# Kernel tuning notes

Hardware: AMD Instinct MI355X
Metric: run time of the kernel (lower is better)

## Reference

```python
import jax, jax.numpy as jnp
import numpy as np

B, T, I = 2048, 256, 64   # batch, seq_len, n_input
H = 128                   # n_lstm_hidden
K = 128                   # n_KDN_hidden
O = 64                    # n_output


def setup_inputs() -> dict:
    key = jax.random.key(0)
    ks = jax.random.split(key, 16)
    def xavier(k, shape):
        fan_in, fan_out = shape[1], shape[0]
        std = np.sqrt(2.0 / (fan_in + fan_out))
        return jax.random.normal(k, shape, dtype=jnp.float32) * std
    inp = {
        'x': jax.random.normal(ks[0], (B, T, I), dtype=jnp.float32),
        # LSTMCell 1 (input I -> hidden H); PyTorch gate order i,f,g,o
        'W_ih1': xavier(ks[1], (4 * H, I)),
        'W_hh1': xavier(ks[2], (4 * H, H)),
        'b_ih1': jnp.zeros((4 * H,), jnp.float32),
        'b_hh1': jnp.zeros((4 * H,), jnp.float32),
        # LSTMCell 2 (H -> H)
        'W_ih2': xavier(ks[3], (4 * H, H)),
        'W_hh2': xavier(ks[4], (4 * H, H)),
        'b_ih2': jnp.zeros((4 * H,), jnp.float32),
        'b_hh2': jnp.zeros((4 * H,), jnp.float32),
        # KDN: 6 Linear layers (H+I)->K, K->K x4, K->O
        'Wk0': xavier(ks[5], (K, H + I)), 'bk0': jnp.zeros((K,), jnp.float32),
        'Wk1': xavier(ks[6], (K, K)),     'bk1': jnp.zeros((K,), jnp.float32),
        'Wk2': xavier(ks[7], (K, K)),     'bk2': jnp.zeros((K,), jnp.float32),
        'Wk3': xavier(ks[8], (K, K)),     'bk3': jnp.zeros((K,), jnp.float32),
        'Wk4': xavier(ks[9], (K, K)),     'bk4': jnp.zeros((K,), jnp.float32),
        'Wk5': xavier(ks[10], (O, K)),    'bk5': jnp.zeros((O,), jnp.float32),
    }
    return inp


def _lstm_cell(x_t, h, c, W_ih, W_hh, b_ih, b_hh):
    # PyTorch LSTMCell math; gates ordered i, f, g, o
    gates = x_t @ W_ih.T + h @ W_hh.T + (b_ih + b_hh)
    i, f, g, o = jnp.split(gates, 4, axis=-1)
    i = jax.nn.sigmoid(i)
    f = jax.nn.sigmoid(f)
    g = jnp.tanh(g)
    o = jax.nn.sigmoid(o)
    c_new = f * c + i * g
    h_new = o * jnp.tanh(c_new)
    return h_new, c_new


def reference(x, W_ih1, W_hh1, b_ih1, b_hh1, W_ih2, W_hh2, b_ih2, b_hh2,
              Wk0, bk0, Wk1, bk1, Wk2, bk2, Wk3, bk3, Wk4, bk4, Wk5, bk5):
    Bx = x.shape[0]
    h1 = jnp.zeros((Bx, H), x.dtype)
    c1 = jnp.zeros((Bx, H), x.dtype)
    h2 = jnp.zeros((Bx, H), x.dtype)
    c2 = jnp.zeros((Bx, H), x.dtype)

    xs = jnp.swapaxes(x, 0, 1)  # [T, B, I] for scan over time

    def step(carry, x_t):
        h1, c1, h2, c2 = carry
        h1, c1 = _lstm_cell(x_t, h1, c1, W_ih1, W_hh1, b_ih1, b_hh1)
        # Dropout is identity in eval mode
        h2, c2 = _lstm_cell(h1, h2, c2, W_ih2, W_hh2, b_ih2, b_hh2)
        return (h1, c1, h2, c2), None

    (h1, c1, h2, c2), _ = jax.lax.scan(step, (h1, c1, h2, c2), xs)

    r = jnp.concatenate([h2, x[:, -1, :]], axis=1)  # [B, H+I]
    y = r
    for W, b in ((Wk0, bk0), (Wk1, bk1), (Wk2, bk2), (Wk3, bk3), (Wk4, bk4)):
        y = jax.nn.relu(y @ W.T + b)
    y = y @ Wk5.T + bk5  # final Linear, no activation
    return (y, h2, r)
```

## Files before the change

kernel.cpp:

```cpp
#include <hip/hip_runtime.h>
#include <cstddef>


typedef __attribute__((ext_vector_type(8))) short short8;
typedef __attribute__((ext_vector_type(4))) float float4v;

#define OFF_Y  ((size_t)0)
#define OFF_H2 ((size_t)2048*64)
#define OFF_R  ((size_t)2048*192)

#define WS_FLAGS   0
#define WS_W1I     64
#define WS_W1H     65600
#define WS_W2I     196672
#define WS_W2H     327744
#define WS_WK0     458816
#define WS_WK1     507968
#define WS_WK2     540736
#define WS_WK3     573504
#define WS_WK4     606272
#define WS_WK5     639040
#define WS_B1      655424
#define WS_B2      657472
#define WS_BK0     659520
#define WS_BK1     660032
#define WS_BK2     660544
#define WS_BK3     661056
#define WS_BK4     661568
#define WS_BK5     662080
#define WS_RB      662336

__device__ __forceinline__ float bf2f(unsigned short u){
  union { unsigned int i; float f; } c; c.i = ((unsigned int)u) << 16; return c.f;
}
__device__ __forceinline__ unsigned short f2bf(float f){
  union { float f; unsigned int i; } c; c.f = f;
  unsigned int x = c.i;
  unsigned int r = (x + 0x7FFFu + ((x >> 16) & 1u)) >> 16;
  return (unsigned short)r;
}

__device__ __forceinline__ float exp2_(float x){
  float r; asm("v_exp_f32 %0, %1" : "=v"(r) : "v"(x)); return r;
}
__device__ __forceinline__ float rcp_(float x){
  float r; asm("v_rcp_f32 %0, %1" : "=v"(r) : "v"(x)); return r;
}
#define LOG2E 1.442695041f
__device__ __forceinline__ float sig_(float x){
  return rcp_(1.0f + exp2_(-LOG2E * x));
}
__device__ __forceinline__ float tanh_(float x){
  return 2.0f * rcp_(1.0f + exp2_(-2.0f*LOG2E * x)) - 1.0f;
}

#define MFMA16(a,b,c) __builtin_amdgcn_mfma_f32_16x16x32_bf16((a),(b),(c),0,0,0)

__device__ __forceinline__ unsigned int ldx2(const void* x, size_t off, int f32){
  if (f32){
    const float* p = (const float*)x + off;
    return (unsigned int)f2bf(p[0]) | ((unsigned int)f2bf(p[1]) << 16);
  }
  return *(const unsigned int*)((const unsigned short*)x + off);
}
__device__ __forceinline__ float ld1f(const void* p, int i, int f32){
  if (f32) return ((const float*)p)[i];
  return bf2f(((const unsigned short*)p)[i]);
}
__device__ __forceinline__ void st1(void* o, size_t off, float v, int f32){
  if (f32) ((float*)o)[off] = v;
  else     ((unsigned short*)o)[off] = f2bf(v);
}

__device__ __forceinline__ void act_cell(const float4v acc[4], float cr[4],
                                         unsigned short hb[4], float hf[4]){
  #pragma unroll
  for (int r = 0; r < 4; r++){
    float ig = sig_(acc[0][r]);
    float fg = sig_(acc[1][r]);
    float gg = tanh_(acc[2][r]);
    float og = sig_(acc[3][r]);
    cr[r] = fg*cr[r] + ig*gg;
    float h = og * tanh_(cr[r]);
    hf[r] = h;
    hb[r] = f2bf(h);
  }
}

__global__ void probe_kernel(const void* x,
                             const void* w1i, const void* w1h,
                             const void* w2i, const void* w2h,
                             const void* k0, const void* k1, const void* k2,
                             const void* k3, const void* k4, const void* k5,
                             int* flags)
{
  const void* arrs[11] = {x, w1i, w1h, w2i, w2h, k0, k1, k2, k3, k4, k5};
  const int lane = threadIdx.x & 63;
  for (int a = 0; a < 11; a++){
    const unsigned short* p = (const unsigned short*)arrs[a];
    int bad = 0;
    #pragma unroll
    for (int j = 0; j < 8; j++){
      float v = bf2f(p[lane*8 + j]);
      if (!(v > -1e3f && v < 1e3f)) bad = 1;
    }
    unsigned long long m = __ballot(bad);
    if (lane == 0) flags[a] = (m != 0ull) ? 1 : 0;
  }
}

__device__ __forceinline__ void conv_range(const void* src, unsigned short* dst,
                                           int lo, int n, int f32, int t){
  int hi = lo + 4096; if (hi > n) hi = n;
  for (int i = lo + t; i < hi; i += 256)
    dst[i] = f32 ? f2bf(((const float*)src)[i]) : ((const unsigned short*)src)[i];
}

__global__ void convert_kernel(const void* w1i, const void* w1h,
                               const void* w2i, const void* w2h,
                               const void* k0, const void* k1, const void* k2,
                               const void* k3, const void* k4, const void* k5,
                               const void* bi1, const void* bh1,
                               const void* bi2, const void* bh2,
                               const void* bb0, const void* bb1, const void* bb2,
                               const void* bb3, const void* bb4, const void* bb5,
                               char* ws)
{
  const int* flags = (const int*)(ws + WS_FLAGS);
  const int b = blockIdx.x, t = threadIdx.x;
  if      (b <  8) conv_range(w1i, (unsigned short*)(ws+WS_W1I), (b-0)*4096, 32768, flags[1], t);
  else if (b < 24) conv_range(w1h, (unsigned short*)(ws+WS_W1H), (b-8)*4096, 65536, flags[2], t);
  else if (b < 40) conv_range(w2i, (unsigned short*)(ws+WS_W2I), (b-24)*4096, 65536, flags[3], t);
  else if (b < 56) conv_range(w2h, (unsigned short*)(ws+WS_W2H), (b-40)*4096, 65536, flags[4], t);
  else if (b < 62) conv_range(k0,  (unsigned short*)(ws+WS_WK0), (b-56)*4096, 24576, flags[5], t);
  else if (b < 66) conv_range(k1,  (unsigned short*)(ws+WS_WK1), (b-62)*4096, 16384, flags[6], t);
  else if (b < 70) conv_range(k2,  (unsigned short*)(ws+WS_WK2), (b-66)*4096, 16384, flags[7], t);
  else if (b < 74) conv_range(k3,  (unsigned short*)(ws+WS_WK3), (b-70)*4096, 16384, flags[8], t);
  else if (b < 78) conv_range(k4,  (unsigned short*)(ws+WS_WK4), (b-74)*4096, 16384, flags[9], t);
  else if (b < 80) conv_range(k5,  (unsigned short*)(ws+WS_WK5), (b-78)*4096,  8192, flags[10], t);
  else {
    float* b1 = (float*)(ws+WS_B1);
    float* b2 = (float*)(ws+WS_B2);
    for (int i = t; i < 512; i += 256){
      b1[i] = ld1f(bi1, i, flags[1]) + ld1f(bh1, i, flags[2]);
      b2[i] = ld1f(bi2, i, flags[3]) + ld1f(bh2, i, flags[4]);
    }
    const void* bks[6] = {bb0, bb1, bb2, bb3, bb4, bb5};
    const size_t dof[6] = {WS_BK0, WS_BK1, WS_BK2, WS_BK3, WS_BK4, WS_BK5};
    for (int a = 0; a < 6; a++){
      int n = (a == 5) ? 64 : 128;
      float* d = (float*)(ws + dof[a]);
      for (int i = t; i < n; i += 256) d[i] = ld1f(bks[a], i, flags[5+a]);
    }
  }
}

__global__ __launch_bounds__(512)
__attribute__((amdgpu_waves_per_eu(2, 2)))
void lstm_kernel(const void* __restrict__ x,
                 const unsigned short* __restrict__ W1I,
                 const unsigned short* __restrict__ W1H,
                 const unsigned short* __restrict__ W2I,
                 const unsigned short* __restrict__ W2H,
                 const float* __restrict__ B1, const float* __restrict__ B2,
                 unsigned short* __restrict__ RB,
                 const int* __restrict__ flags,
                 void* __restrict__ out)
{
  __shared__ __align__(16) short8 WPARK[8][16][64];
  __shared__ __align__(16) unsigned short A1s[2][16][200];
  __shared__ __align__(16) unsigned short A2s[2][16][264];

  const int fx = flags[0];
  const int fo = fx;

  const int tid  = threadIdx.x;
  const int w    = tid >> 6;
  const int lane = tid & 63;
  const int l15  = lane & 15;
  const int lq   = lane >> 4;
  const int r0   = blockIdx.x * 16;
  const int mycol = w*16 + l15;
  const int xm = tid >> 5;
  const int xc = (tid & 31) * 2;

  #pragma unroll
  for (int q = 0; q < 4; q++){
    const int n = q*128 + mycol;
    WPARK[w][q*4+0][lane] = *(const short8*)(W1I + (size_t)n*64 + lq*8);
    WPARK[w][q*4+1][lane] = *(const short8*)(W1I + (size_t)n*64 + 32 + lq*8);
    WPARK[w][q*4+2][lane] = *(const short8*)(W1H + (size_t)n*128 + lq*8);
    WPARK[w][q*4+3][lane] = *(const short8*)(W1H + (size_t)n*128 + 32 + lq*8);
  }

  short8 w1r[4][2];
  #pragma unroll
  for (int q = 0; q < 4; q++){
    const int n = q*128 + mycol;
    #pragma unroll
    for (int i = 0; i < 2; i++)
      w1r[q][i] = *(const short8*)(W1H + (size_t)n*128 + (i+2)*32 + lq*8);
  }
  short8 w2r[4][8];
  #pragma unroll
  for (int q = 0; q < 4; q++){
    const int n = q*128 + mycol;
    #pragma unroll
    for (int kc = 0; kc < 8; kc++){
      const unsigned short* p = (kc < 4) ? (W2I + (size_t)n*128 + kc*32     + lq*8)
                                         : (W2H + (size_t)n*128 + (kc-4)*32 + lq*8);
      w2r[q][kc] = *(const short8*)p;
    }
  }
  #pragma unroll
  for (int q = 0; q < 4; q++){
    #pragma unroll
    for (int i = 0; i < 2; i++)  asm volatile("" : "+v"(w1r[q][i]));
    #pragma unroll
    for (int kc = 0; kc < 8; kc++) asm volatile("" : "+v"(w2r[q][kc]));
  }

  float b1[4], b2[4];
  #pragma unroll
  for (int q = 0; q < 4; q++){
    b1[q] = B1[q*128 + mycol];
    b2[q] = B2[q*128 + mycol];
  }

  for (int i = tid; i < 16*128; i += 512){
    int m = i >> 7, c = i & 127;
    A1s[0][m][64 + c]  = 0;
    A2s[0][m][128 + c] = 0;
  }
  size_t xoff = ((size_t)(r0 + xm))*256*64 + xc;
  *(unsigned int*)&A1s[0][xm][xc] = ldx2(x, xoff, fx);
  unsigned int xv1 = ldx2(x, xoff + 64,  fx);
  unsigned int xv_c = ldx2(x, xoff + 128, fx);
  xoff += 128;

  float c1r[4] = {0.f,0.f,0.f,0.f};
  float c2r[4] = {0.f,0.f,0.f,0.f};
  float h2f[4] = {0.f,0.f,0.f,0.f};
  unsigned short h2b[4] = {0,0,0,0};
  __syncthreads();

  {
    float4v acc1[4];
    #pragma unroll
    for (int q = 0; q < 4; q++) acc1[q] = (float4v){b1[q], b1[q], b1[q], b1[q]};
    #pragma unroll
    for (int kc = 0; kc < 4; kc++){
      short8 af = *(const short8*)&A1s[0][l15][kc*32 + lq*8];
      #pragma unroll
      for (int q = 0; q < 4; q++)
        acc1[q] = MFMA16(af, WPARK[w][q*4+kc][lane], acc1[q]);
    }
    #pragma unroll
    for (int kc = 4; kc < 6; kc++){
      short8 af = *(const short8*)&A1s[0][l15][kc*32 + lq*8];
      #pragma unroll
      for (int q = 0; q < 4; q++)
        acc1[q] = MFMA16(af, w1r[q][kc-4], acc1[q]);
    }
    float h1f[4]; unsigned short h1b[4];
    act_cell(acc1, c1r, h1b, h1f);
    #pragma unroll
    for (int r = 0; r < 4; r++){
      int row = lq*4 + r;
      A2s[0][row][mycol]      = h1b[r];
      A1s[1][row][64 + mycol] = h1b[r];
    }
    *(unsigned int*)&A1s[1][xm][xc] = xv1;
  }
  __syncthreads();

  for (int t = 0; t < 256; t++){
    const int rA = t & 1;
    const int rB = rA ^ 1;

    unsigned int xv_n = 0u;
    if (t < 253){
      xoff += 64;
      xv_n = ldx2(x, xoff, fx);
    }

    float4v acc2[4];
    #pragma unroll
    for (int q = 0; q < 4; q++) acc2[q] = (float4v){b2[q], b2[q], b2[q], b2[q]};
    #pragma unroll
    for (int kc = 0; kc < 8; kc++){
      short8 af = *(const short8*)&A2s[rA][l15][kc*32 + lq*8];
      acc2[0] = MFMA16(af, w2r[0][kc], acc2[0]);
      acc2[1] = MFMA16(af, w2r[1][kc], acc2[1]);
      acc2[2] = MFMA16(af, w2r[2][kc], acc2[2]);
      acc2[3] = MFMA16(af, w2r[3][kc], acc2[3]);
    }

    if (t < 255){
      float4v acc1[4];
      #pragma unroll
      for (int q = 0; q < 4; q++) acc1[q] = (float4v){b1[q], b1[q], b1[q], b1[q]};
      #pragma unroll
      for (int kc = 0; kc < 4; kc++){
        short8 af = *(const short8*)&A1s[rB][l15][kc*32 + lq*8];
        #pragma unroll
        for (int q = 0; q < 4; q++)
          acc1[q] = MFMA16(af, WPARK[w][q*4+kc][lane], acc1[q]);
      }
      #pragma unroll
      for (int kc = 4; kc < 6; kc++){
        short8 af = *(const short8*)&A1s[rB][l15][kc*32 + lq*8];
        #pragma unroll
        for (int q = 0; q < 4; q++)
          acc1[q] = MFMA16(af, w1r[q][kc-4], acc1[q]);
      }

      act_cell(acc2, c2r, h2b, h2f);
      #pragma unroll
      for (int r = 0; r < 4; r++)
        A2s[rB][lq*4 + r][128 + mycol] = h2b[r];

      float h1f[4]; unsigned short h1b[4];
      act_cell(acc1, c1r, h1b, h1f);
      #pragma unroll
      for (int r = 0; r < 4; r++){
        int row = lq*4 + r;
        A2s[rB][row][mycol]      = h1b[r];
        A1s[rA][row][64 + mycol] = h1b[r];
      }
      *(unsigned int*)&A1s[rA][xm][xc] = xv_c;
      xv_c = xv_n;
    } else {
      act_cell(acc2, c2r, h2b, h2f);
    }
    __syncthreads();
  }

  #pragma unroll
  for (int r = 0; r < 4; r++){
    size_t grow = (size_t)(r0 + lq*4 + r);
    st1(out, OFF_H2 + grow*128 + mycol, h2f[r], fo);
    st1(out, OFF_R  + grow*192 + mycol, h2f[r], fo);
    RB[grow*192 + mycol] = h2b[r];
  }
  {
    float v0, v1;
    if (fx){ const float* p = (const float*)x + xoff; v0 = p[0]; v1 = p[1]; }
    else   { const unsigned short* p = (const unsigned short*)x + xoff;
             v0 = bf2f(p[0]); v1 = bf2f(p[1]); }
    size_t rrow = (size_t)(r0 + xm)*192 + 128 + xc;
    st1(out, OFF_R + rrow,     v0, fo);
    st1(out, OFF_R + rrow + 1, v1, fo);
    RB[rrow]     = f2bf(v0);
    RB[rrow + 1] = f2bf(v1);
  }
}

__global__ __launch_bounds__(256)
void kdn_kernel(const char* __restrict__ ws, void* __restrict__ out)
{
  __shared__ __align__(16) unsigned short bufA[16][200];
  __shared__ __align__(16) unsigned short bufB[16][200];

  const int* flags = (const int*)(ws + WS_FLAGS);
  const int fo = flags[0];

  const int tid = threadIdx.x;
  const int w    = tid >> 6;
  const int lane = tid & 63;
  const int l15  = lane & 15;
  const int lq   = lane >> 4;
  const int r0  = blockIdx.x * 16;

  const unsigned short* RB = (const unsigned short*)(ws + WS_RB);

  for (int i = tid; i < 1536; i += 256){
    int row = i / 96, c2 = (i % 96) * 2;
    *(unsigned int*)&bufA[row][c2] =
        *(const unsigned int*)&RB[(size_t)(r0 + row)*192 + c2];
  }
  __syncthreads();

  const unsigned short* WK[6] = {
    (const unsigned short*)(ws+WS_WK0), (const unsigned short*)(ws+WS_WK1),
    (const unsigned short*)(ws+WS_WK2), (const unsigned short*)(ws+WS_WK3),
    (const unsigned short*)(ws+WS_WK4), (const unsigned short*)(ws+WS_WK5)};
  const float* BK[6] = {
    (const float*)(ws+WS_BK0), (const float*)(ws+WS_BK1),
    (const float*)(ws+WS_BK2), (const float*)(ws+WS_BK3),
    (const float*)(ws+WS_BK4), (const float*)(ws+WS_BK5)};

  unsigned short (*src)[200] = bufA;
  unsigned short (*dst)[200] = bufB;

  #pragma unroll
  for (int l = 0; l < 5; l++){
    const int K = (l == 0) ? 192 : 128;
    const int nk = K / 32;
    #pragma unroll
    for (int tau = 0; tau < 2; tau++){
      const int n = w*32 + tau*16 + l15;
      float bv = BK[l][n];
      float4v acc = {bv, bv, bv, bv};
      for (int kc = 0; kc < nk; kc++){
        short8 af = *(const short8*)&src[l15][kc*32 + lq*8];
        short8 wf = *(const short8*)(WK[l] + (size_t)n*K + kc*32 + lq*8);
        acc = MFMA16(af, wf, acc);
      }
      #pragma unroll
      for (int r = 0; r < 4; r++)
        dst[lq*4 + r][n] = f2bf(fmaxf(acc[r], 0.0f));
    }
    __syncthreads();
    unsigned short (*tmp)[200] = src; src = dst; dst = tmp;
  }

  {
    const int n = w*16 + l15;
    float bv = BK[5][n];
    float4v acc = {bv, bv, bv, bv};
    #pragma unroll
    for (int kc = 0; kc < 4; kc++){
      short8 af = *(const short8*)&src[l15][kc*32 + lq*8];
      short8 wf = *(const short8*)(WK[5] + (size_t)n*128 + kc*32 + lq*8);
      acc = MFMA16(af, wf, acc);
    }
    #pragma unroll
    for (int r = 0; r < 4; r++)
      st1(out, OFF_Y + (size_t)(r0 + lq*4 + r)*64 + n, acc[r], fo);
  }
}

extern "C" void kernel_launch(void* const* d_in, const int* in_sizes, int n_in,
                              void* d_out, int out_size, void* d_ws, size_t ws_size,
                              hipStream_t stream)
{
  (void)in_sizes; (void)n_in; (void)ws_size; (void)out_size;

  const void* x    = d_in[0];
  const void* Wih1 = d_in[1];
  const void* Whh1 = d_in[2];
  const void* bih1 = d_in[3];
  const void* bhh1 = d_in[4];
  const void* Wih2 = d_in[5];
  const void* Whh2 = d_in[6];
  const void* bih2 = d_in[7];
  const void* bhh2 = d_in[8];
  const void* Wk0 = d_in[9];  const void* bk0 = d_in[10];
  const void* Wk1 = d_in[11]; const void* bk1 = d_in[12];
  const void* Wk2 = d_in[13]; const void* bk2 = d_in[14];
  const void* Wk3 = d_in[15]; const void* bk3 = d_in[16];
  const void* Wk4 = d_in[17]; const void* bk4 = d_in[18];
  const void* Wk5 = d_in[19]; const void* bk5 = d_in[20];

  char* ws = (char*)d_ws;

  hipLaunchKernelGGL(probe_kernel, dim3(1), dim3(64), 0, stream,
                     x, Wih1, Whh1, Wih2, Whh2,
                     Wk0, Wk1, Wk2, Wk3, Wk4, Wk5, (int*)(ws + WS_FLAGS));
  hipLaunchKernelGGL(convert_kernel, dim3(81), dim3(256), 0, stream,
                     Wih1, Whh1, Wih2, Whh2,
                     Wk0, Wk1, Wk2, Wk3, Wk4, Wk5,
                     bih1, bhh1, bih2, bhh2,
                     bk0, bk1, bk2, bk3, bk4, bk5, ws);
  hipLaunchKernelGGL(lstm_kernel, dim3(128), dim3(512), 0, stream,
                     x,
                     (const unsigned short*)(ws + WS_W1I),
                     (const unsigned short*)(ws + WS_W1H),
                     (const unsigned short*)(ws + WS_W2I),
                     (const unsigned short*)(ws + WS_W2H),
                     (const float*)(ws + WS_B1), (const float*)(ws + WS_B2),
                     (unsigned short*)(ws + WS_RB),
                     (const int*)(ws + WS_FLAGS),
                     d_out);
  hipLaunchKernelGGL(kdn_kernel, dim3(128), dim3(256), 0, stream,
                     ws, d_out);
}
```

Baseline: 962.2 us.

## Split LSTM K-reduction across two wave halves with LDS partial-sum exchange

The LSTM block grows from 512 to 1024 threads, and each column group's K dimension is split between two wave halves. Partial MFMA accumulators are exchanged through LDS, and cell-2 and cell-1 activations are divided between the halves. This removes the LDS-parked weights and halves each wave's serial MFMA chain per timestep, at the cost of an extra barrier and LDS round trip per step. The KDN kernel also moves to 8 rows per block on 256 blocks, padding the unused rows with zeros.

```diff
diff --git a/kernel.cpp b/kernel.cpp
--- a/kernel.cpp
+++ b/kernel.cpp
@@ -155,8 +155,8 @@
   }
 }
 
-__global__ __launch_bounds__(512)
-__attribute__((amdgpu_waves_per_eu(2, 2)))
+__global__ __launch_bounds__(1024)
+__attribute__((amdgpu_waves_per_eu(4, 4)))
 void lstm_kernel(const void* __restrict__ x,
                  const unsigned short* __restrict__ W1I,
                  const unsigned short* __restrict__ W1H,
@@ -167,9 +167,10 @@
                  const int* __restrict__ flags,
                  void* __restrict__ out)
 {
-  __shared__ __align__(16) short8 WPARK[8][16][64];
   __shared__ __align__(16) unsigned short A1s[2][16][200];
   __shared__ __align__(16) unsigned short A2s[2][16][264];
+  __shared__ __align__(16) float4v PS1[8][4][64];
+  __shared__ __align__(16) float4v PS2[8][4][64];
 
   const int fx = flags[0];
   const int fo = fx;
@@ -179,64 +180,67 @@
   const int lane = tid & 63;
   const int l15  = lane & 15;
   const int lq   = lane >> 4;
+  const int cg   = w & 7;
+  const int kh   = w >> 3;
   const int r0   = blockIdx.x * 16;
-  const int mycol = w*16 + l15;
+  const int mycol = cg*16 + l15;
   const int xm = tid >> 5;
   const int xc = (tid & 31) * 2;
 
+  short8 w1r[4][3];
   #pragma unroll
   for (int q = 0; q < 4; q++){
     const int n = q*128 + mycol;
-    WPARK[w][q*4+0][lane] = *(const short8*)(W1I + (size_t)n*64 + lq*8);
-    WPARK[w][q*4+1][lane] = *(const short8*)(W1I + (size_t)n*64 + 32 + lq*8);
-    WPARK[w][q*4+2][lane] = *(const short8*)(W1H + (size_t)n*128 + lq*8);
-    WPARK[w][q*4+3][lane] = *(const short8*)(W1H + (size_t)n*128 + 32 + lq*8);
-  }
-
-  short8 w1r[4][2];
+    #pragma unroll
+    for (int k = 0; k < 3; k++){
+      const int gk = kh*3 + k;
+      const unsigned short* p;
+      if      (gk == 0) p = W1I + (size_t)n*64 + lq*8;
+      else if (gk == 1) p = W1I + (size_t)n*64 + 32 + lq*8;
+      else              p = W1H + (size_t)n*128 + (gk-2)*32 + lq*8;
+      w1r[q][k] = *(const short8*)p;
+    }
+  }
+  short8 w2r[4][4];
   #pragma unroll
   for (int q = 0; q < 4; q++){
     const int n = q*128 + mycol;
     #pragma unroll
-    for (int i = 0; i < 2; i++)
-      w1r[q][i] = *(const short8*)(W1H + (size_t)n*128 + (i+2)*32 + lq*8);
-  }
-  short8 w2r[4][8];
+    for (int k = 0; k < 4; k++){
+      const int gk = kh*4 + k;
+      const unsigned short* p = (gk < 4) ? (W2I + (size_t)n*128 + gk*32     + lq*8)
+                                         : (W2H + (size_t)n*128 + (gk-4)*32 + lq*8);
+      w2r[q][k] = *(const short8*)p;
+    }
+  }
   #pragma unroll
   for (int q = 0; q < 4; q++){
-    const int n = q*128 + mycol;
-    #pragma unroll
-    for (int kc = 0; kc < 8; kc++){
-      const unsigned short* p = (kc < 4) ? (W2I + (size_t)n*128 + kc*32     + lq*8)
-                                         : (W2H + (size_t)n*128 + (kc-4)*32 + lq*8);
-      w2r[q][kc] = *(const short8*)p;
-    }
-  }
-  #pragma unroll
-  for (int q = 0; q < 4; q++){
-    #pragma unroll
-    for (int i = 0; i < 2; i++)  asm volatile("" : "+v"(w1r[q][i]));
-    #pragma unroll
-    for (int kc = 0; kc < 8; kc++) asm volatile("" : "+v"(w2r[q][kc]));
+    #pragma unroll
+    for (int k = 0; k < 3; k++) asm volatile("" : "+v"(w1r[q][k]));
+    #pragma unroll
+    for (int k = 0; k < 4; k++) asm volatile("" : "+v"(w2r[q][k]));
   }
 
   float b1[4], b2[4];
   #pragma unroll
   for (int q = 0; q < 4; q++){
-    b1[q] = B1[q*128 + mycol];
-    b2[q] = B2[q*128 + mycol];
-  }
-
-  for (int i = tid; i < 16*128; i += 512){
+    b1[q] = kh ? 0.0f : B1[q*128 + mycol];
+    b2[q] = kh ? 0.0f : B2[q*128 + mycol];
+  }
+
+  for (int i = tid; i < 16*128; i += 1024){
     int m = i >> 7, c = i & 127;
     A1s[0][m][64 + c]  = 0;
     A2s[0][m][128 + c] = 0;
   }
-  size_t xoff = ((size_t)(r0 + xm))*256*64 + xc;
-  *(unsigned int*)&A1s[0][xm][xc] = ldx2(x, xoff, fx);
-  unsigned int xv1 = ldx2(x, xoff + 64,  fx);
-  unsigned int xv_c = ldx2(x, xoff + 128, fx);
-  xoff += 128;
+  size_t xoff = ((size_t)(r0 + (xm & 15)))*256*64 + xc;
+  unsigned int xv1 = 0u, xv_c = 0u;
+  if (tid < 512){
+    *(unsigned int*)&A1s[0][xm][xc] = ldx2(x, xoff, fx);
+    xv1  = ldx2(x, xoff + 64,  fx);
+    xv_c = ldx2(x, xoff + 128, fx);
+    xoff += 128;
+  }
 
   float c1r[4] = {0.f,0.f,0.f,0.f};
   float c2r[4] = {0.f,0.f,0.f,0.f};
@@ -249,37 +253,40 @@
     #pragma unroll
     for (int q = 0; q < 4; q++) acc1[q] = (float4v){b1[q], b1[q], b1[q], b1[q]};
     #pragma unroll
-    for (int kc = 0; kc < 4; kc++){
-      short8 af = *(const short8*)&A1s[0][l15][kc*32 + lq*8];
+    for (int k = 0; k < 3; k++){
+      const int gk = kh*3 + k;
+      short8 af = *(const short8*)&A1s[0][l15][gk*32 + lq*8];
       #pragma unroll
       for (int q = 0; q < 4; q++)
-        acc1[q] = MFMA16(af, WPARK[w][q*4+kc][lane], acc1[q]);
-    }
-    #pragma unroll
-    for (int kc = 4; kc < 6; kc++){
-      short8 af = *(const short8*)&A1s[0][l15][kc*32 + lq*8];
-      #pragma unroll
-      for (int q = 0; q < 4; q++)
-        acc1[q] = MFMA16(af, w1r[q][kc-4], acc1[q]);
-    }
-    float h1f[4]; unsigned short h1b[4];
-    act_cell(acc1, c1r, h1b, h1f);
-    #pragma unroll
-    for (int r = 0; r < 4; r++){
-      int row = lq*4 + r;
-      A2s[0][row][mycol]      = h1b[r];
-      A1s[1][row][64 + mycol] = h1b[r];
-    }
-    *(unsigned int*)&A1s[1][xm][xc] = xv1;
-  }
-  __syncthreads();
+        acc1[q] = MFMA16(af, w1r[q][k], acc1[q]);
+    }
+    if (kh == 1){
+      #pragma unroll
+      for (int q = 0; q < 4; q++) PS1[cg][q][lane] = acc1[q];
+    }
+    __syncthreads();
+    if (kh == 0){
+      #pragma unroll
+      for (int q = 0; q < 4; q++) acc1[q] += PS1[cg][q][lane];
+      float h1f[4]; unsigned short h1b[4];
+      act_cell(acc1, c1r, h1b, h1f);
+      #pragma unroll
+      for (int r = 0; r < 4; r++){
+        int row = lq*4 + r;
+        A2s[0][row][mycol]      = h1b[r];
+        A1s[1][row][64 + mycol] = h1b[r];
+      }
+      if (tid < 512) *(unsigned int*)&A1s[1][xm][xc] = xv1;
+    }
+    __syncthreads();
+  }
 
   for (int t = 0; t < 256; t++){
     const int rA = t & 1;
     const int rB = rA ^ 1;
 
     unsigned int xv_n = 0u;
-    if (t < 253){
+    if (t < 253 && tid < 512){
       xoff += 64;
       xv_n = ldx2(x, xoff, fx);
     }
@@ -288,38 +295,48 @@
     #pragma unroll
     for (int q = 0; q < 4; q++) acc2[q] = (float4v){b2[q], b2[q], b2[q], b2[q]};
     #pragma unroll
-    for (int kc = 0; kc < 8; kc++){
-      short8 af = *(const short8*)&A2s[rA][l15][kc*32 + lq*8];
-      acc2[0] = MFMA16(af, w2r[0][kc], acc2[0]);
-      acc2[1] = MFMA16(af, w2r[1][kc], acc2[1]);
-      acc2[2] = MFMA16(af, w2r[2][kc], acc2[2]);
-      acc2[3] = MFMA16(af, w2r[3][kc], acc2[3]);
-    }
-
+    for (int k = 0; k < 4; k++){
+      const int gk = kh*4 + k;
+      short8 af = *(const short8*)&A2s[rA][l15][gk*32 + lq*8];
+      acc2[0] = MFMA16(af, w2r[0][k], acc2[0]);
+      acc2[1] = MFMA16(af, w2r[1][k], acc2[1]);
+      acc2[2] = MFMA16(af, w2r[2][k], acc2[2]);
+      acc2[3] = MFMA16(af, w2r[3][k], acc2[3]);
+    }
+
+    float4v acc1[4];
     if (t < 255){
-      float4v acc1[4];
       #pragma unroll
       for (int q = 0; q < 4; q++) acc1[q] = (float4v){b1[q], b1[q], b1[q], b1[q]};
       #pragma unroll
-      for (int kc = 0; kc < 4; kc++){
-        short8 af = *(const short8*)&A1s[rB][l15][kc*32 + lq*8];
+      for (int k = 0; k < 3; k++){
+        const int gk = kh*3 + k;
+        short8 af = *(const short8*)&A1s[rB][l15][gk*32 + lq*8];
         #pragma unroll
         for (int q = 0; q < 4; q++)
-          acc1[q] = MFMA16(af, WPARK[w][q*4+kc][lane], acc1[q]);
+          acc1[q] = MFMA16(af, w1r[q][k], acc1[q]);
       }
-      #pragma unroll
-      for (int kc = 4; kc < 6; kc++){
-        short8 af = *(const short8*)&A1s[rB][l15][kc*32 + lq*8];
-        #pragma unroll
-        for (int q = 0; q < 4; q++)
-          acc1[q] = MFMA16(af, w1r[q][kc-4], acc1[q]);
-      }
-
+    }
+
+    if (kh == 0){
+      #pragma unroll
+      for (int q = 0; q < 4; q++) PS2[cg][q][lane] = acc2[q];
+    } else if (t < 255){
+      #pragma unroll
+      for (int q = 0; q < 4; q++) PS1[cg][q][lane] = acc1[q];
+    }
+    __syncthreads();
+
+    if (kh == 1){
+      #pragma unroll
+      for (int q = 0; q < 4; q++) acc2[q] += PS2[cg][q][lane];
       act_cell(acc2, c2r, h2b, h2f);
       #pragma unroll
       for (int r = 0; r < 4; r++)
         A2s[rB][lq*4 + r][128 + mycol] = h2b[r];
-
+    } else if (t < 255){
+      #pragma unroll
+      for (int q = 0; q < 4; q++) acc1[q] += PS1[cg][q][lane];
       float h1f[4]; unsigned short h1b[4];
       act_cell(acc1, c1r, h1b, h1f);
       #pragma unroll
@@ -328,22 +345,21 @@
         A2s[rB][row][mycol]      = h1b[r];
         A1s[rA][row][64 + mycol] = h1b[r];
       }
-      *(unsigned int*)&A1s[rA][xm][xc] = xv_c;
-      xv_c = xv_n;
-    } else {
-      act_cell(acc2, c2r, h2b, h2f);
-    }
+      if (tid < 512) *(unsigned int*)&A1s[rA][xm][xc] = xv_c;
+    }
+    xv_c = xv_n;
     __syncthreads();
   }
 
-  #pragma unroll
-  for (int r = 0; r < 4; r++){
-    size_t grow = (size_t)(r0 + lq*4 + r);
-    st1(out, OFF_H2 + grow*128 + mycol, h2f[r], fo);
-    st1(out, OFF_R  + grow*192 + mycol, h2f[r], fo);
-    RB[grow*192 + mycol] = h2b[r];
-  }
-  {
+  if (kh == 1){
+    #pragma unroll
+    for (int r = 0; r < 4; r++){
+      size_t grow = (size_t)(r0 + lq*4 + r);
+      st1(out, OFF_H2 + grow*128 + mycol, h2f[r], fo);
+      st1(out, OFF_R  + grow*192 + mycol, h2f[r], fo);
+      RB[grow*192 + mycol] = h2b[r];
+    }
+  } else {
     float v0, v1;
     if (fx){ const float* p = (const float*)x + xoff; v0 = p[0]; v1 = p[1]; }
     else   { const unsigned short* p = (const unsigned short*)x + xoff;
@@ -370,14 +386,18 @@
   const int lane = tid & 63;
   const int l15  = lane & 15;
   const int lq   = lane >> 4;
-  const int r0  = blockIdx.x * 16;
+  const int r0  = blockIdx.x * 8;
 
   const unsigned short* RB = (const unsigned short*)(ws + WS_RB);
 
-  for (int i = tid; i < 1536; i += 256){
+  for (int i = tid; i < 768; i += 256){
     int row = i / 96, c2 = (i % 96) * 2;
     *(unsigned int*)&bufA[row][c2] =
         *(const unsigned int*)&RB[(size_t)(r0 + row)*192 + c2];
+  }
+  for (int i = tid; i < 768; i += 256){
+    int row = 8 + i / 96, c2 = (i % 96) * 2;
+    *(unsigned int*)&bufA[row][c2] = 0u;
   }
   __syncthreads();
 
@@ -426,8 +446,11 @@
       acc = MFMA16(af, wf, acc);
     }
     #pragma unroll
-    for (int r = 0; r < 4; r++)
-      st1(out, OFF_Y + (size_t)(r0 + lq*4 + r)*64 + n, acc[r], fo);
+    for (int r = 0; r < 4; r++){
+      int row = lq*4 + r;
+      if (row < 8)
+        st1(out, OFF_Y + (size_t)(r0 + row)*64 + n, acc[r], fo);
+    }
   }
 }
 
@@ -463,7 +486,7 @@
                      Wk0, Wk1, Wk2, Wk3, Wk4, Wk5,
                      bih1, bhh1, bih2, bhh2,
                      bk0, bk1, bk2, bk3, bk4, bk5, ws);
-  hipLaunchKernelGGL(lstm_kernel, dim3(128), dim3(512), 0, stream,
+  hipLaunchKernelGGL(lstm_kernel, dim3(128), dim3(1024), 0, stream,
                      x,
                      (const unsigned short*)(ws + WS_W1I),
                      (const unsigned short*)(ws + WS_W1H),
@@ -473,6 +496,6 @@
                      (unsigned short*)(ws + WS_RB),
                      (const int*)(ws + WS_FLAGS),
                      d_out);
-  hipLaunchKernelGGL(kdn_kernel, dim3(128), dim3(256), 0, stream,
+  hipLaunchKernelGGL(kdn_kernel, dim3(256), dim3(256), 0, stream,
                      ws, d_out);
 }
```

After: 3.454 ms. 3.59x slower.

## Fuse KDN MLP into LSTM kernel tail and use packed bf16 conversion

Applied to the files above, without the earlier changes.

The separate KDN kernel is folded into the end of the LSTM kernel: the final h2 and last x row are written into reused shared memory instead of a global bf16 buffer, and the six linear layers then run in-block with 8 waves, each computing one 16-column tile. This removes a kernel launch and a global round trip of the concatenated state. It also replaces the software bf16 rounding with the hardware packed convert instruction in the activation cell and the x loading. The cost is an extra barrier per layer, so the block's shared tiles can be overwritten safely.

```diff
diff --git a/kernel.cpp b/kernel.cpp
--- a/kernel.cpp
+++ b/kernel.cpp
@@ -28,7 +28,6 @@
 #define WS_BK3     661056
 #define WS_BK4     661568
 #define WS_BK5     662080
-#define WS_RB      662336
 
 __device__ __forceinline__ float bf2f(unsigned short u){
   union { unsigned int i; float f; } c; c.i = ((unsigned int)u) << 16; return c.f;
@@ -39,6 +38,11 @@
   unsigned int r = (x + 0x7FFFu + ((x >> 16) & 1u)) >> 16;
   return (unsigned short)r;
 }
+__device__ __forceinline__ unsigned int cvtpk(float lo, float hi){
+  unsigned int r;
+  asm("v_cvt_pk_bf16_f32 %0, %1, %2" : "=v"(r) : "v"(lo), "v"(hi));
+  return r;
+}
 
 __device__ __forceinline__ float exp2_(float x){
   float r; asm("v_exp_f32 %0, %1" : "=v"(r) : "v"(x)); return r;
@@ -59,7 +63,7 @@
 __device__ __forceinline__ unsigned int ldx2(const void* x, size_t off, int f32){
   if (f32){
     const float* p = (const float*)x + off;
-    return (unsigned int)f2bf(p[0]) | ((unsigned int)f2bf(p[1]) << 16);
+    return cvtpk(p[0], p[1]);
   }
   return *(const unsigned int*)((const unsigned short*)x + off);
 }
@@ -81,10 +85,12 @@
     float gg = tanh_(acc[2][r]);
     float og = sig_(acc[3][r]);
     cr[r] = fg*cr[r] + ig*gg;
-    float h = og * tanh_(cr[r]);
-    hf[r] = h;
-    hb[r] = f2bf(h);
-  }
+    hf[r] = og * tanh_(cr[r]);
+  }
+  unsigned int p0 = cvtpk(hf[0], hf[1]);
+  unsigned int p1 = cvtpk(hf[2], hf[3]);
+  hb[0] = (unsigned short)p0;  hb[1] = (unsigned short)(p0 >> 16);
+  hb[2] = (unsigned short)p1;  hb[3] = (unsigned short)(p1 >> 16);
 }
 
 __global__ void probe_kernel(const void* x,
@@ -158,15 +164,17 @@
 __global__ __launch_bounds__(512)
 __attribute__((amdgpu_waves_per_eu(2, 2)))
 void lstm_kernel(const void* __restrict__ x,
-                 const unsigned short* __restrict__ W1I,
-                 const unsigned short* __restrict__ W1H,
-                 const unsigned short* __restrict__ W2I,
-                 const unsigned short* __restrict__ W2H,
-                 const float* __restrict__ B1, const float* __restrict__ B2,
-                 unsigned short* __restrict__ RB,
-                 const int* __restrict__ flags,
+                 const char* __restrict__ ws,
                  void* __restrict__ out)
 {
+  const unsigned short* W1I = (const unsigned short*)(ws + WS_W1I);
+  const unsigned short* W1H = (const unsigned short*)(ws + WS_W1H);
+  const unsigned short* W2I = (const unsigned short*)(ws + WS_W2I);
+  const unsigned short* W2H = (const unsigned short*)(ws + WS_W2H);
+  const float* B1 = (const float*)(ws + WS_B1);
+  const float* B2 = (const float*)(ws + WS_B2);
+  const int* flags = (const int*)(ws + WS_FLAGS);
+
   __shared__ __align__(16) short8 WPARK[8][16][64];
   __shared__ __align__(16) unsigned short A1s[2][16][200];
   __shared__ __align__(16) unsigned short A2s[2][16][264];
@@ -336,12 +344,15 @@
     __syncthreads();
   }
 
+  unsigned short (*kA)[200] = (unsigned short (*)[200])&WPARK[0][0][0];
+  unsigned short (*kB)[200] = (unsigned short (*)[200])(((char*)&WPARK[0][0][0]) + 6400);
+
   #pragma unroll
   for (int r = 0; r < 4; r++){
     size_t grow = (size_t)(r0 + lq*4 + r);
     st1(out, OFF_H2 + grow*128 + mycol, h2f[r], fo);
     st1(out, OFF_R  + grow*192 + mycol, h2f[r], fo);
-    RB[grow*192 + mycol] = h2b[r];
+    kA[lq*4 + r][mycol] = h2b[r];
   }
   {
     float v0, v1;
@@ -351,33 +362,9 @@
     size_t rrow = (size_t)(r0 + xm)*192 + 128 + xc;
     st1(out, OFF_R + rrow,     v0, fo);
     st1(out, OFF_R + rrow + 1, v1, fo);
-    RB[rrow]     = f2bf(v0);
-    RB[rrow + 1] = f2bf(v1);
-  }
-}
-
-__global__ __launch_bounds__(256)
-void kdn_kernel(const char* __restrict__ ws, void* __restrict__ out)
-{
-  __shared__ __align__(16) unsigned short bufA[16][200];
-  __shared__ __align__(16) unsigned short bufB[16][200];
-
-  const int* flags = (const int*)(ws + WS_FLAGS);
-  const int fo = flags[0];
-
-  const int tid = threadIdx.x;
-  const int w    = tid >> 6;
-  const int lane = tid & 63;
-  const int l15  = lane & 15;
-  const int lq   = lane >> 4;
-  const int r0  = blockIdx.x * 16;
-
-  const unsigned short* RB = (const unsigned short*)(ws + WS_RB);
-
-  for (int i = tid; i < 1536; i += 256){
-    int row = i / 96, c2 = (i % 96) * 2;
-    *(unsigned int*)&bufA[row][c2] =
-        *(const unsigned int*)&RB[(size_t)(r0 + row)*192 + c2];
+    unsigned int xpk = cvtpk(v0, v1);
+    kA[xm][128 + xc]     = (unsigned short)xpk;
+    kA[xm][128 + xc + 1] = (unsigned short)(xpk >> 16);
   }
   __syncthreads();
 
@@ -390,32 +377,30 @@
     (const float*)(ws+WS_BK2), (const float*)(ws+WS_BK3),
     (const float*)(ws+WS_BK4), (const float*)(ws+WS_BK5)};
 
-  unsigned short (*src)[200] = bufA;
-  unsigned short (*dst)[200] = bufB;
+  unsigned short (*src)[200] = kA;
+  unsigned short (*dst)[200] = kB;
 
   #pragma unroll
   for (int l = 0; l < 5; l++){
     const int K = (l == 0) ? 192 : 128;
     const int nk = K / 32;
-    #pragma unroll
-    for (int tau = 0; tau < 2; tau++){
-      const int n = w*32 + tau*16 + l15;
-      float bv = BK[l][n];
-      float4v acc = {bv, bv, bv, bv};
-      for (int kc = 0; kc < nk; kc++){
-        short8 af = *(const short8*)&src[l15][kc*32 + lq*8];
-        short8 wf = *(const short8*)(WK[l] + (size_t)n*K + kc*32 + lq*8);
-        acc = MFMA16(af, wf, acc);
-      }
-      #pragma unroll
-      for (int r = 0; r < 4; r++)
-        dst[lq*4 + r][n] = f2bf(fmaxf(acc[r], 0.0f));
-    }
+    const int n = mycol;
+    float bv = BK[l][n];
+    float4v acc = {bv, bv, bv, bv};
+    for (int kc = 0; kc < nk; kc++){
+      short8 af = *(const short8*)&src[l15][kc*32 + lq*8];
+      short8 wf = *(const short8*)(WK[l] + (size_t)n*K + kc*32 + lq*8);
+      acc = MFMA16(af, wf, acc);
+    }
+    __syncthreads();
+    #pragma unroll
+    for (int r = 0; r < 4; r++)
+      dst[lq*4 + r][n] = f2bf(fmaxf(acc[r], 0.0f));
     __syncthreads();
     unsigned short (*tmp)[200] = src; src = dst; dst = tmp;
   }
 
-  {
+  if (w < 4){
     const int n = w*16 + l15;
     float bv = BK[5][n];
     float4v acc = {bv, bv, bv, bv};
@@ -464,15 +449,5 @@
                      bih1, bhh1, bih2, bhh2,
                      bk0, bk1, bk2, bk3, bk4, bk5, ws);
   hipLaunchKernelGGL(lstm_kernel, dim3(128), dim3(512), 0, stream,
-                     x,
-                     (const unsigned short*)(ws + WS_W1I),
-                     (const unsigned short*)(ws + WS_W1H),
-                     (const unsigned short*)(ws + WS_W2I),
-                     (const unsigned short*)(ws + WS_W2H),
-                     (const float*)(ws + WS_B1), (const float*)(ws + WS_B2),
-                     (unsigned short*)(ws + WS_RB),
-                     (const int*)(ws + WS_FLAGS),
-                     d_out);
-  hipLaunchKernelGGL(kdn_kernel, dim3(128), dim3(256), 0, stream,
-                     ws, d_out);
-}
+                     x, (const char*)ws, d_out);
+}
```

Result: no change. 972.6 us (+1.1%).
